# Kernel tuning notes

Measured on AMD Instinct MI355X. Metric: run time of the kernel, lower is better.

The kernel has to match this reference:

```python
import jax, jax.numpy as jnp
import numpy as np

EMB_DIM = 1024
ATTN_DIM = 1024


def setup_inputs() -> dict:
    key = jax.random.key(0)
    k_x, k_wk, k_wq, k_wv = jax.random.split(key, 4)
    bound = 1.0 / np.sqrt(EMB_DIM)  # nn.Linear default init range
    return {
        "embedded": jax.random.normal(k_x, (4, 2048, EMB_DIM), dtype=jnp.float32),
        "W_k": jax.random.uniform(k_wk, (ATTN_DIM, EMB_DIM), jnp.float32, -bound, bound),
        "W_q": jax.random.uniform(k_wq, (ATTN_DIM, EMB_DIM), jnp.float32, -bound, bound),
        "W_v": jax.random.uniform(k_wv, (ATTN_DIM, EMB_DIM), jnp.float32, -bound, bound),
    }


def reference(embedded, W_k, W_q, W_v):
    # Linear (bias=False): y = x @ W.T
    K = jnp.einsum("bse,ae->bsa", embedded, W_k)
    Q = jnp.einsum("bse,ae->bsa", embedded, W_q)
    V = jnp.einsum("bse,ae->bsa", embedded, W_v)
    S = K.shape[1]
    scale = 1.0 / jnp.sqrt(jnp.float32(ATTN_DIM))
    scores = jnp.einsum("bqa,bka->bqk", Q, K) * scale  # [B, S, S]
    causal = jnp.tril(jnp.ones((S, S), dtype=bool))  # True = keep
    scores = jnp.where(causal[None, :, :], scores, -jnp.inf)
    attn = jax.nn.softmax(scores, axis=2)
    out = jnp.einsum("bqk,bka->bqa", attn, V)
    # torch.round(x, decimals=4)
    return jnp.round(out * 1e4) / 1e4
```

## Files before the change

kernel.cpp:

```cpp
#include <hip/hip_runtime.h>
#include <stdint.h>

#define B_ 4
#define S_ 2048
#define E_ 1024
#define D_ 1024

typedef short  bf16x8 __attribute__((ext_vector_type(8)));
typedef float  f32x4  __attribute__((ext_vector_type(4)));

static __device__ __forceinline__ unsigned short f2bf(float f) {
    unsigned int u = __float_as_uint(f);
    u += 0x7fffu + ((u >> 16) & 1u);
    return (unsigned short)(u >> 16);
}

static __device__ __forceinline__ void async16(const unsigned short* g, unsigned short* l) {
    auto gp = (const __attribute__((address_space(1))) void*)(uintptr_t)g;
    auto lp = (__attribute__((address_space(3))) void*)(uintptr_t)l;
    __builtin_amdgcn_global_load_lds(gp, lp, 16, 0, 0);
}


__global__ __launch_bounds__(256)
void convert_kernel(const float* __restrict__ x,  const float* __restrict__ Wk,
                    const float* __restrict__ Wq, const float* __restrict__ Wv,
                    unsigned short* __restrict__ xb, unsigned short* __restrict__ Wb)
{
    const long long idx = ((long long)blockIdx.x * 256 + threadIdx.x) * 4;
    const float* src; unsigned short* dst; long long off;
    if (idx < (long long)B_ * S_ * E_) {
        src = x; dst = xb; off = idx;
    } else {
        long long w = idx - (long long)B_ * S_ * E_;
        const int sel = (int)(w >> 20);
        off = w & 1048575LL;
        src = (sel == 0) ? Wk : (sel == 1) ? Wq : Wv;
        dst = Wb + ((long long)sel << 20);
    }
    const float4 f = *(const float4*)(src + off);
    ushort4 u = { f2bf(f.x), f2bf(f.y), f2bf(f.z), f2bf(f.w) };
    *(ushort4*)(dst + off) = u;
}

__global__ __launch_bounds__(256, 4)
void proj_kernel(const unsigned short* __restrict__ xb,
                 const unsigned short* __restrict__ Wb,
                 unsigned short* __restrict__ Qb,
                 unsigned short* __restrict__ Kb,
                 unsigned short* __restrict__ Vt)
{
    __shared__ __align__(16) unsigned short As[128 * 64];
    __shared__ __align__(16) unsigned short Bs[128 * 64];

    const int t    = threadIdx.x;
    const int ny   = blockIdx.x;
    const int m0   = blockIdx.y * 128;
    const int wsel = ny >> 3;
    const int nloc = (ny & 7) * 128;

    const int lane = t & 63, wave = t >> 6;
    const int l15 = lane & 15, quad = lane >> 4;
    const int wm = wave & 1, wn = wave >> 1;
    const int sr = lane >> 3;
    const int sq = ((lane & 7) ^ sr) * 8;
    const int l7 = l15 & 7;
    const int rcA0 = (wm * 64 + l15) * 64 + ((quad ^ l7) * 8);
    const int rcA1 = (wm * 64 + l15) * 64 + (((4 + quad) ^ l7) * 8);
    const int rcB0 = (wn * 64 + l15) * 64 + ((quad ^ l7) * 8);
    const int rcB1 = (wn * 64 + l15) * 64 + (((4 + quad) ^ l7) * 8);

    const unsigned short* gA = xb + (size_t)(m0 + wave * 32 + sr) * E_ + sq;
    const unsigned short* gB = Wb + (size_t)(ny * 128 + wave * 32 + sr) * E_ + sq;
    unsigned short* lA = &As[wave * 2048];
    unsigned short* lB = &Bs[wave * 2048];

    f32x4 acc[4][4];
    #pragma unroll
    for (int i = 0; i < 4; i++)
        #pragma unroll
        for (int j = 0; j < 4; j++) acc[i][j] = {0.f, 0.f, 0.f, 0.f};

    for (int k0 = 0; k0 < E_; k0 += 64) {
        __syncthreads();
        #pragma unroll
        for (int i = 0; i < 4; i++) {
            async16(gA + k0 + i * 8 * E_, lA + i * 512);
            async16(gB + k0 + i * 8 * E_, lB + i * 512);
        }
        __syncthreads();

        #pragma unroll
        for (int s = 0; s < 2; s++) {
            bf16x8 af[4], bfr[4];
            const int ra = s ? rcA1 : rcA0, rb = s ? rcB1 : rcB0;
            #pragma unroll
            for (int i = 0; i < 4; i++) af[i]  = *(const bf16x8*)&As[ra + i * 1024];
            #pragma unroll
            for (int j = 0; j < 4; j++) bfr[j] = *(const bf16x8*)&Bs[rb + j * 1024];
            #pragma unroll
            for (int i = 0; i < 4; i++)
                #pragma unroll
                for (int j = 0; j < 4; j++)
                    acc[i][j] = __builtin_amdgcn_mfma_f32_16x16x32_bf16(af[i], bfr[j], acc[i][j], 0, 0, 0);
        }
    }

    if (wsel == 0) {
        #pragma unroll
        for (int i = 0; i < 4; i++)
            #pragma unroll
            for (int j = 0; j < 4; j++) {
                const int gn = nloc + wn * 64 + j * 16 + l15;
                #pragma unroll
                for (int r = 0; r < 4; r++) {
                    const int gm = m0 + wm * 64 + i * 16 + quad * 4 + r;
                    Kb[(size_t)gm * D_ + gn] = f2bf(acc[i][j][r]);
                }
            }
    } else if (wsel == 1) {
        #pragma unroll
        for (int i = 0; i < 4; i++)
            #pragma unroll
            for (int j = 0; j < 4; j++) {
                const int gn = nloc + wn * 64 + j * 16 + l15;
                #pragma unroll
                for (int r = 0; r < 4; r++) {
                    const int gm = m0 + wm * 64 + i * 16 + quad * 4 + r;
                    Qb[(size_t)gm * D_ + gn] = f2bf(acc[i][j][r] * 0.03125f);
                }
            }
    } else {
        #pragma unroll
        for (int i = 0; i < 4; i++)
            #pragma unroll
            for (int j = 0; j < 4; j++) {
                const int s0 = m0 + wm * 64 + i * 16 + quad * 4;
                const int b  = s0 >> 11, sl = s0 & (S_ - 1);
                const int gn = nloc + wn * 64 + j * 16 + l15;
                ushort4 u = { f2bf(acc[i][j][0]), f2bf(acc[i][j][1]),
                              f2bf(acc[i][j][2]), f2bf(acc[i][j][3]) };
                *(ushort4*)&Vt[((size_t)(b << 10) + gn) * S_ + sl] = u;
            }
    }
}

__global__ __launch_bounds__(256, 4)
void expscores_kernel(const unsigned short* __restrict__ Qb,
                      const unsigned short* __restrict__ Kb,
                      unsigned short* __restrict__ P,
                      float* __restrict__ rowpart)
{
    const int nt = blockIdx.x;
    const int mt = 15 - blockIdx.y;
    const int b  = blockIdx.z;
    if (nt > mt) return;

    __shared__ __align__(16) unsigned short As[128 * 64];
    __shared__ __align__(16) unsigned short Bs[128 * 64];

    const int t = threadIdx.x;
    const int m0 = mt * 128, n0 = nt * 128;

    const int lane = t & 63, wave = t >> 6;
    const int l15 = lane & 15, quad = lane >> 4;
    const int wm = wave & 1, wn = wave >> 1;
    const int sr = lane >> 3;
    const int sq = ((lane & 7) ^ sr) * 8;
    const int l7 = l15 & 7;
    const int rcA0 = (wm * 64 + l15) * 64 + ((quad ^ l7) * 8);
    const int rcA1 = (wm * 64 + l15) * 64 + (((4 + quad) ^ l7) * 8);
    const int rcB0 = (wn * 64 + l15) * 64 + ((quad ^ l7) * 8);
    const int rcB1 = (wn * 64 + l15) * 64 + (((4 + quad) ^ l7) * 8);

    const unsigned short* gA = Qb + (size_t)b * S_ * D_ + (size_t)(m0 + wave * 32 + sr) * D_ + sq;
    const unsigned short* gB = Kb + (size_t)b * S_ * D_ + (size_t)(n0 + wave * 32 + sr) * D_ + sq;
    unsigned short* lA = &As[wave * 2048];
    unsigned short* lB = &Bs[wave * 2048];

    f32x4 acc[4][4];
    #pragma unroll
    for (int i = 0; i < 4; i++)
        #pragma unroll
        for (int j = 0; j < 4; j++) acc[i][j] = {0.f, 0.f, 0.f, 0.f};

    for (int k0 = 0; k0 < D_; k0 += 64) {
        __syncthreads();
        #pragma unroll
        for (int i = 0; i < 4; i++) {
            async16(gA + k0 + i * 8 * D_, lA + i * 512);
            async16(gB + k0 + i * 8 * D_, lB + i * 512);
        }
        __syncthreads();

        #pragma unroll
        for (int s = 0; s < 2; s++) {
            bf16x8 af[4], bfr[4];
            const int ra = s ? rcA1 : rcA0, rb = s ? rcB1 : rcB0;
            #pragma unroll
            for (int i = 0; i < 4; i++) af[i]  = *(const bf16x8*)&As[ra + i * 1024];
            #pragma unroll
            for (int j = 0; j < 4; j++) bfr[j] = *(const bf16x8*)&Bs[rb + j * 1024];
            #pragma unroll
            for (int i = 0; i < 4; i++)
                #pragma unroll
                for (int j = 0; j < 4; j++)
                    acc[i][j] = __builtin_amdgcn_mfma_f32_16x16x32_bf16(af[i], bfr[j], acc[i][j], 0, 0, 0);
        }
    }

    unsigned short* Pb = P + (size_t)b * S_ * S_;
    #pragma unroll
    for (int i = 0; i < 4; i++)
        #pragma unroll
        for (int j = 0; j < 4; j++) {
            const int gn = n0 + wn * 64 + j * 16 + l15;
            #pragma unroll
            for (int r = 0; r < 4; r++) {
                const int gm = m0 + wm * 64 + i * 16 + quad * 4 + r;
                const float e = (gn <= gm) ? __expf(acc[i][j][r]) : 0.f;
                acc[i][j][r] = e;
                Pb[(size_t)gm * S_ + gn] = f2bf(e);
            }
        }

    float* rp = rowpart + ((size_t)b * 32 + nt * 2 + wn) * S_;
    #pragma unroll
    for (int i = 0; i < 4; i++) {
        float rsub[4];
        #pragma unroll
        for (int r = 0; r < 4; r++) {
            float s = acc[i][0][r] + acc[i][1][r] + acc[i][2][r] + acc[i][3][r];
            #pragma unroll
            for (int off = 8; off; off >>= 1) s += __shfl_xor(s, off);
            rsub[r] = s;
        }
        if (l15 == 0) {
            #pragma unroll
            for (int r = 0; r < 4; r++)
                rp[m0 + wm * 64 + i * 16 + quad * 4 + r] = rsub[r];
        }
    }
}

__global__ __launch_bounds__(256, 4)
void pv_kernel(const unsigned short* __restrict__ P,
               const unsigned short* __restrict__ Vt,
               const float* __restrict__ rowpart,
               float* __restrict__ out)
{
    const int nt = blockIdx.x;
    const int mt = 15 - blockIdx.y;
    const int b  = blockIdx.z;

    __shared__ __align__(16) unsigned short As[128 * 64];
    __shared__ __align__(16) unsigned short Bs[128 * 64];

    const int t = threadIdx.x;
    const int m0 = mt * 128, n0 = nt * 128;
    const int kend = m0 + 128;

    const int lane = t & 63, wave = t >> 6;
    const int l15 = lane & 15, quad = lane >> 4;
    const int wm = wave & 1, wn = wave >> 1;
    const int sr = lane >> 3;
    const int sq = ((lane & 7) ^ sr) * 8;
    const int l7 = l15 & 7;
    const int rcA0 = (wm * 64 + l15) * 64 + ((quad ^ l7) * 8);
    const int rcA1 = (wm * 64 + l15) * 64 + (((4 + quad) ^ l7) * 8);
    const int rcB0 = (wn * 64 + l15) * 64 + ((quad ^ l7) * 8);
    const int rcB1 = (wn * 64 + l15) * 64 + (((4 + quad) ^ l7) * 8);

    const unsigned short* gA = P  + (size_t)b * S_ * S_ + (size_t)(m0 + wave * 32 + sr) * S_ + sq;
    const unsigned short* gB = Vt + (size_t)b * D_ * S_ + (size_t)(n0 + wave * 32 + sr) * S_ + sq;
    unsigned short* lA = &As[wave * 2048];
    unsigned short* lB = &Bs[wave * 2048];

    f32x4 acc[4][4];
    #pragma unroll
    for (int i = 0; i < 4; i++)
        #pragma unroll
        for (int j = 0; j < 4; j++) acc[i][j] = {0.f, 0.f, 0.f, 0.f};

    for (int k0 = 0; k0 < kend; k0 += 64) {
        __syncthreads();
        #pragma unroll
        for (int i = 0; i < 4; i++) {
            async16(gA + k0 + i * 8 * S_, lA + i * 512);
            async16(gB + k0 + i * 8 * S_, lB + i * 512);
        }
        __syncthreads();

        #pragma unroll
        for (int s = 0; s < 2; s++) {
            bf16x8 af[4], bfr[4];
            const int ra = s ? rcA1 : rcA0, rb = s ? rcB1 : rcB0;
            #pragma unroll
            for (int i = 0; i < 4; i++) af[i]  = *(const bf16x8*)&As[ra + i * 1024];
            #pragma unroll
            for (int j = 0; j < 4; j++) bfr[j] = *(const bf16x8*)&Bs[rb + j * 1024];
            #pragma unroll
            for (int i = 0; i < 4; i++)
                #pragma unroll
                for (int j = 0; j < 4; j++)
                    acc[i][j] = __builtin_amdgcn_mfma_f32_16x16x32_bf16(af[i], bfr[j], acc[i][j], 0, 0, 0);
        }
    }

    const int nsl = 2 * mt + 2;
    const float* rp = rowpart + (size_t)b * 32 * S_ + (m0 + wm * 64 + lane);
    float rsum = 0.f;
    for (int k = 0; k < nsl; k++) rsum += rp[(size_t)k * S_];
    const float invr = 1.0f / rsum;

    #pragma unroll
    for (int i = 0; i < 4; i++) {
        #pragma unroll
        for (int r = 0; r < 4; r++) {
            const float vr = __shfl(invr, i * 16 + quad * 4 + r);
            const int gm = m0 + wm * 64 + i * 16 + quad * 4 + r;
            #pragma unroll
            for (int j = 0; j < 4; j++) {
                const int gn = n0 + wn * 64 + j * 16 + l15;
                out[((size_t)b * S_ + gm) * D_ + gn] = rintf(acc[i][j][r] * vr * 1e4f) * 1e-4f;
            }
        }
    }
}

extern "C" void kernel_launch(void* const* d_in, const int* in_sizes, int n_in,
                              void* d_out, int out_size, void* d_ws, size_t ws_size,
                              hipStream_t stream)
{
    (void)in_sizes; (void)n_in; (void)out_size; (void)ws_size;
    const float* x  = (const float*)d_in[0];
    const float* Wk = (const float*)d_in[1];
    const float* Wq = (const float*)d_in[2];
    const float* Wv = (const float*)d_in[3];
    float* out = (float*)d_out;

    char* ws = (char*)d_ws;
    unsigned short* Qb = (unsigned short*)ws;
    unsigned short* Kb = Qb + (size_t)B_ * S_ * D_;
    unsigned short* Vt = Kb + (size_t)B_ * S_ * D_;
    unsigned short* P  = Vt + (size_t)B_ * D_ * S_;
    unsigned short* xb = P;
    unsigned short* Wb = xb + (size_t)B_ * S_ * E_;
    float* rowpart = (float*)(P + (size_t)B_ * S_ * S_);

    const int conv_blocks = (B_ * S_ * E_ + 3 * D_ * E_) / (256 * 4);
    convert_kernel  <<<conv_blocks, 256, 0, stream>>>(x, Wk, Wq, Wv, xb, Wb);
    proj_kernel     <<<dim3(24, 64, 1),   256, 0, stream>>>(xb, Wb, Qb, Kb, Vt);
    expscores_kernel<<<dim3(16, 16, B_),  256, 0, stream>>>(Qb, Kb, P, rowpart);
    pv_kernel       <<<dim3(8, 16, B_),   256, 0, stream>>>(P, Vt, rowpart, out);
}
```

Measured before the change: 228.5 us.

## Shrink attention tiles to 64 rows and swap projection grid order

The score and PV kernels now use 64x128 tiles with 4 waves each covering 32 columns instead of 128x128 tiles, and the rowpart layout grows from 32 to 64 partial slices per row. This aims to cut wasted work on diagonal causal tiles and to give more, smaller blocks for better load balance across CUs. The cost is lower arithmetic intensity per block and more partial-sum traffic. The projection kernel's grid is also transposed so that consecutive blocks walk M rather than weight-column tiles, which changes L2 reuse of the operands.

Result: slower. 242.3 us (+6.1%).

```diff
diff --git a/kernel.cpp b/kernel.cpp
--- a/kernel.cpp
+++ b/kernel.cpp
@@ -54,8 +54,8 @@
     __shared__ __align__(16) unsigned short Bs[128 * 64];
 
     const int t    = threadIdx.x;
-    const int ny   = blockIdx.x;
-    const int m0   = blockIdx.y * 128;
+    const int m0   = blockIdx.x * 128;
+    const int ny   = blockIdx.y;
     const int wsel = ny >> 3;
     const int nloc = (ny & 7) * 128;
 
@@ -152,59 +152,58 @@
                       float* __restrict__ rowpart)
 {
     const int nt = blockIdx.x;
-    const int mt = 15 - blockIdx.y;
+    const int mt = 31 - blockIdx.y;
     const int b  = blockIdx.z;
-    if (nt > mt) return;
-
-    __shared__ __align__(16) unsigned short As[128 * 64];
+    if (nt > (mt >> 1)) return;
+
+    __shared__ __align__(16) unsigned short As[64 * 64];
     __shared__ __align__(16) unsigned short Bs[128 * 64];
 
     const int t = threadIdx.x;
-    const int m0 = mt * 128, n0 = nt * 128;
+    const int m0 = mt * 64, n0 = nt * 128;
 
     const int lane = t & 63, wave = t >> 6;
     const int l15 = lane & 15, quad = lane >> 4;
-    const int wm = wave & 1, wn = wave >> 1;
+    const int wn = wave;
     const int sr = lane >> 3;
     const int sq = ((lane & 7) ^ sr) * 8;
     const int l7 = l15 & 7;
-    const int rcA0 = (wm * 64 + l15) * 64 + ((quad ^ l7) * 8);
-    const int rcA1 = (wm * 64 + l15) * 64 + (((4 + quad) ^ l7) * 8);
-    const int rcB0 = (wn * 64 + l15) * 64 + ((quad ^ l7) * 8);
-    const int rcB1 = (wn * 64 + l15) * 64 + (((4 + quad) ^ l7) * 8);
-
-    const unsigned short* gA = Qb + (size_t)b * S_ * D_ + (size_t)(m0 + wave * 32 + sr) * D_ + sq;
+
+    const unsigned short* gA = Qb + (size_t)b * S_ * D_ + (size_t)(m0 + wave * 16 + sr) * D_ + sq;
     const unsigned short* gB = Kb + (size_t)b * S_ * D_ + (size_t)(n0 + wave * 32 + sr) * D_ + sq;
-    unsigned short* lA = &As[wave * 2048];
+    unsigned short* lA = &As[wave * 1024];
     unsigned short* lB = &Bs[wave * 2048];
 
-    f32x4 acc[4][4];
+    f32x4 acc[4][2];
     #pragma unroll
     for (int i = 0; i < 4; i++)
         #pragma unroll
-        for (int j = 0; j < 4; j++) acc[i][j] = {0.f, 0.f, 0.f, 0.f};
+        for (int j = 0; j < 2; j++) acc[i][j] = {0.f, 0.f, 0.f, 0.f};
 
     for (int k0 = 0; k0 < D_; k0 += 64) {
         __syncthreads();
         #pragma unroll
-        for (int i = 0; i < 4; i++) {
+        for (int i = 0; i < 2; i++)
             async16(gA + k0 + i * 8 * D_, lA + i * 512);
+        #pragma unroll
+        for (int i = 0; i < 4; i++)
             async16(gB + k0 + i * 8 * D_, lB + i * 512);
-        }
         __syncthreads();
 
         #pragma unroll
         for (int s = 0; s < 2; s++) {
-            bf16x8 af[4], bfr[4];
-            const int ra = s ? rcA1 : rcA0, rb = s ? rcB1 : rcB0;
-            #pragma unroll
-            for (int i = 0; i < 4; i++) af[i]  = *(const bf16x8*)&As[ra + i * 1024];
-            #pragma unroll
-            for (int j = 0; j < 4; j++) bfr[j] = *(const bf16x8*)&Bs[rb + j * 1024];
-            #pragma unroll
-            for (int i = 0; i < 4; i++)
-                #pragma unroll
-                for (int j = 0; j < 4; j++)
+            bf16x8 af[4], bfr[2];
+            const int cs = (s * 4 + quad);
+            #pragma unroll
+            for (int i = 0; i < 4; i++)
+                af[i] = *(const bf16x8*)&As[(i * 16 + l15) * 64 + ((cs ^ l7) * 8)];
+            #pragma unroll
+            for (int j = 0; j < 2; j++)
+                bfr[j] = *(const bf16x8*)&Bs[(wn * 32 + j * 16 + l15) * 64 + ((cs ^ l7) * 8)];
+            #pragma unroll
+            for (int i = 0; i < 4; i++)
+                #pragma unroll
+                for (int j = 0; j < 2; j++)
                     acc[i][j] = __builtin_amdgcn_mfma_f32_16x16x32_bf16(af[i], bfr[j], acc[i][j], 0, 0, 0);
         }
     }
@@ -213,24 +212,24 @@
     #pragma unroll
     for (int i = 0; i < 4; i++)
         #pragma unroll
-        for (int j = 0; j < 4; j++) {
-            const int gn = n0 + wn * 64 + j * 16 + l15;
+        for (int j = 0; j < 2; j++) {
+            const int gn = n0 + wn * 32 + j * 16 + l15;
             #pragma unroll
             for (int r = 0; r < 4; r++) {
-                const int gm = m0 + wm * 64 + i * 16 + quad * 4 + r;
+                const int gm = m0 + i * 16 + quad * 4 + r;
                 const float e = (gn <= gm) ? __expf(acc[i][j][r]) : 0.f;
                 acc[i][j][r] = e;
                 Pb[(size_t)gm * S_ + gn] = f2bf(e);
             }
         }
 
-    float* rp = rowpart + ((size_t)b * 32 + nt * 2 + wn) * S_;
+    float* rp = rowpart + ((size_t)b * 64 + nt * 4 + wn) * S_;
     #pragma unroll
     for (int i = 0; i < 4; i++) {
         float rsub[4];
         #pragma unroll
         for (int r = 0; r < 4; r++) {
-            float s = acc[i][0][r] + acc[i][1][r] + acc[i][2][r] + acc[i][3][r];
+            float s = acc[i][0][r] + acc[i][1][r];
             #pragma unroll
             for (int off = 8; off; off >>= 1) s += __shfl_xor(s, off);
             rsub[r] = s;
@@ -238,7 +237,7 @@
         if (l15 == 0) {
             #pragma unroll
             for (int r = 0; r < 4; r++)
-                rp[m0 + wm * 64 + i * 16 + quad * 4 + r] = rsub[r];
+                rp[m0 + i * 16 + quad * 4 + r] = rsub[r];
         }
     }
 }
@@ -250,65 +249,64 @@
                float* __restrict__ out)
 {
     const int nt = blockIdx.x;
-    const int mt = 15 - blockIdx.y;
+    const int mt = 31 - blockIdx.y;
     const int b  = blockIdx.z;
 
-    __shared__ __align__(16) unsigned short As[128 * 64];
+    __shared__ __align__(16) unsigned short As[64 * 64];
     __shared__ __align__(16) unsigned short Bs[128 * 64];
 
     const int t = threadIdx.x;
-    const int m0 = mt * 128, n0 = nt * 128;
-    const int kend = m0 + 128;
+    const int m0 = mt * 64, n0 = nt * 128;
+    const int kend = m0 + 64;
 
     const int lane = t & 63, wave = t >> 6;
     const int l15 = lane & 15, quad = lane >> 4;
-    const int wm = wave & 1, wn = wave >> 1;
+    const int wn = wave;
     const int sr = lane >> 3;
     const int sq = ((lane & 7) ^ sr) * 8;
     const int l7 = l15 & 7;
-    const int rcA0 = (wm * 64 + l15) * 64 + ((quad ^ l7) * 8);
-    const int rcA1 = (wm * 64 + l15) * 64 + (((4 + quad) ^ l7) * 8);
-    const int rcB0 = (wn * 64 + l15) * 64 + ((quad ^ l7) * 8);
-    const int rcB1 = (wn * 64 + l15) * 64 + (((4 + quad) ^ l7) * 8);
-
-    const unsigned short* gA = P  + (size_t)b * S_ * S_ + (size_t)(m0 + wave * 32 + sr) * S_ + sq;
+
+    const unsigned short* gA = P  + (size_t)b * S_ * S_ + (size_t)(m0 + wave * 16 + sr) * S_ + sq;
     const unsigned short* gB = Vt + (size_t)b * D_ * S_ + (size_t)(n0 + wave * 32 + sr) * S_ + sq;
-    unsigned short* lA = &As[wave * 2048];
+    unsigned short* lA = &As[wave * 1024];
     unsigned short* lB = &Bs[wave * 2048];
 
-    f32x4 acc[4][4];
+    f32x4 acc[4][2];
     #pragma unroll
     for (int i = 0; i < 4; i++)
         #pragma unroll
-        for (int j = 0; j < 4; j++) acc[i][j] = {0.f, 0.f, 0.f, 0.f};
+        for (int j = 0; j < 2; j++) acc[i][j] = {0.f, 0.f, 0.f, 0.f};
 
     for (int k0 = 0; k0 < kend; k0 += 64) {
         __syncthreads();
         #pragma unroll
-        for (int i = 0; i < 4; i++) {
+        for (int i = 0; i < 2; i++)
             async16(gA + k0 + i * 8 * S_, lA + i * 512);
+        #pragma unroll
+        for (int i = 0; i < 4; i++)
             async16(gB + k0 + i * 8 * S_, lB + i * 512);
-        }
         __syncthreads();
 
         #pragma unroll
         for (int s = 0; s < 2; s++) {
-            bf16x8 af[4], bfr[4];
-            const int ra = s ? rcA1 : rcA0, rb = s ? rcB1 : rcB0;
-            #pragma unroll
-            for (int i = 0; i < 4; i++) af[i]  = *(const bf16x8*)&As[ra + i * 1024];
-            #pragma unroll
-            for (int j = 0; j < 4; j++) bfr[j] = *(const bf16x8*)&Bs[rb + j * 1024];
-            #pragma unroll
-            for (int i = 0; i < 4; i++)
-                #pragma unroll
-                for (int j = 0; j < 4; j++)
+            bf16x8 af[4], bfr[2];
+            const int cs = (s * 4 + quad);
+            #pragma unroll
+            for (int i = 0; i < 4; i++)
+                af[i] = *(const bf16x8*)&As[(i * 16 + l15) * 64 + ((cs ^ l7) * 8)];
+            #pragma unroll
+            for (int j = 0; j < 2; j++)
+                bfr[j] = *(const bf16x8*)&Bs[(wn * 32 + j * 16 + l15) * 64 + ((cs ^ l7) * 8)];
+            #pragma unroll
+            for (int i = 0; i < 4; i++)
+                #pragma unroll
+                for (int j = 0; j < 2; j++)
                     acc[i][j] = __builtin_amdgcn_mfma_f32_16x16x32_bf16(af[i], bfr[j], acc[i][j], 0, 0, 0);
         }
     }
 
-    const int nsl = 2 * mt + 2;
-    const float* rp = rowpart + (size_t)b * 32 * S_ + (m0 + wm * 64 + lane);
+    const int nsl = ((mt >> 1) + 1) * 4;
+    const float* rp = rowpart + (size_t)b * 64 * S_ + (m0 + lane);
     float rsum = 0.f;
     for (int k = 0; k < nsl; k++) rsum += rp[(size_t)k * S_];
     const float invr = 1.0f / rsum;
@@ -318,10 +316,10 @@
         #pragma unroll
         for (int r = 0; r < 4; r++) {
             const float vr = __shfl(invr, i * 16 + quad * 4 + r);
-            const int gm = m0 + wm * 64 + i * 16 + quad * 4 + r;
-            #pragma unroll
-            for (int j = 0; j < 4; j++) {
-                const int gn = n0 + wn * 64 + j * 16 + l15;
+            const int gm = m0 + i * 16 + quad * 4 + r;
+            #pragma unroll
+            for (int j = 0; j < 2; j++) {
+                const int gn = n0 + wn * 32 + j * 16 + l15;
                 out[((size_t)b * S_ + gm) * D_ + gn] = rintf(acc[i][j][r] * vr * 1e4f) * 1e-4f;
             }
         }
@@ -350,7 +348,7 @@
 
     const int conv_blocks = (B_ * S_ * E_ + 3 * D_ * E_) / (256 * 4);
     convert_kernel  <<<conv_blocks, 256, 0, stream>>>(x, Wk, Wq, Wv, xb, Wb);
-    proj_kernel     <<<dim3(24, 64, 1),   256, 0, stream>>>(xb, Wb, Qb, Kb, Vt);
-    expscores_kernel<<<dim3(16, 16, B_),  256, 0, stream>>>(Qb, Kb, P, rowpart);
-    pv_kernel       <<<dim3(8, 16, B_),   256, 0, stream>>>(P, Vt, rowpart, out);
-}
+    proj_kernel     <<<dim3(64, 24, 1),   256, 0, stream>>>(xb, Wb, Qb, Kb, Vt);
+    expscores_kernel<<<dim3(16, 32, B_),  256, 0, stream>>>(Qb, Kb, P, rowpart);
+    pv_kernel       <<<dim3(8, 32, B_),   256, 0, stream>>>(P, Vt, rowpart, out);
+}
```

## Widen score and PV tiles to 128x256 and reorder projection grid

Applied to the files above, without the earlier changes.

The exp-scores and PV kernels now use 128x256 output tiles per block, with each wave computing a 64x128 sub-tile (32 accumulators). This halves the number of blocks and raises MFMA work per LDS fragment load. Row partial sums are re-indexed to 16 slices per batch, and occupancy hints drop to 2 blocks per CU. The projection grid is transposed so consecutive blocks walk M rather than N, and the expscores row order is no longer reversed. In exchange the kernels need more registers and LDS and run fewer blocks, and the 256-wide causal tiles compute more masked-out work on the diagonal.

Result: no change. 232.6 us (+1.8%).

```diff
diff --git a/kernel.cpp b/kernel.cpp
--- a/kernel.cpp
+++ b/kernel.cpp
@@ -54,8 +54,8 @@
     __shared__ __align__(16) unsigned short Bs[128 * 64];
 
     const int t    = threadIdx.x;
-    const int ny   = blockIdx.x;
-    const int m0   = blockIdx.y * 128;
+    const int m0   = blockIdx.x * 128;
+    const int ny   = blockIdx.y;
     const int wsel = ny >> 3;
     const int nloc = (ny & 7) * 128;
 
@@ -145,22 +145,22 @@
     }
 }
 
-__global__ __launch_bounds__(256, 4)
+__global__ __launch_bounds__(256, 2)
 void expscores_kernel(const unsigned short* __restrict__ Qb,
                       const unsigned short* __restrict__ Kb,
                       unsigned short* __restrict__ P,
                       float* __restrict__ rowpart)
 {
     const int nt = blockIdx.x;
-    const int mt = 15 - blockIdx.y;
+    const int mt = blockIdx.y;
     const int b  = blockIdx.z;
-    if (nt > mt) return;
+    if (nt > (mt >> 1)) return;
 
     __shared__ __align__(16) unsigned short As[128 * 64];
-    __shared__ __align__(16) unsigned short Bs[128 * 64];
+    __shared__ __align__(16) unsigned short Bs[256 * 64];
 
     const int t = threadIdx.x;
-    const int m0 = mt * 128, n0 = nt * 128;
+    const int m0 = mt * 128, n0 = nt * 256;
 
     const int lane = t & 63, wave = t >> 6;
     const int l15 = lane & 15, quad = lane >> 4;
@@ -168,43 +168,42 @@
     const int sr = lane >> 3;
     const int sq = ((lane & 7) ^ sr) * 8;
     const int l7 = l15 & 7;
-    const int rcA0 = (wm * 64 + l15) * 64 + ((quad ^ l7) * 8);
-    const int rcA1 = (wm * 64 + l15) * 64 + (((4 + quad) ^ l7) * 8);
-    const int rcB0 = (wn * 64 + l15) * 64 + ((quad ^ l7) * 8);
-    const int rcB1 = (wn * 64 + l15) * 64 + (((4 + quad) ^ l7) * 8);
 
     const unsigned short* gA = Qb + (size_t)b * S_ * D_ + (size_t)(m0 + wave * 32 + sr) * D_ + sq;
-    const unsigned short* gB = Kb + (size_t)b * S_ * D_ + (size_t)(n0 + wave * 32 + sr) * D_ + sq;
+    const unsigned short* gB = Kb + (size_t)b * S_ * D_ + (size_t)(n0 + wave * 64 + sr) * D_ + sq;
     unsigned short* lA = &As[wave * 2048];
-    unsigned short* lB = &Bs[wave * 2048];
-
-    f32x4 acc[4][4];
+    unsigned short* lB = &Bs[wave * 4096];
+
+    f32x4 acc[4][8];
     #pragma unroll
     for (int i = 0; i < 4; i++)
         #pragma unroll
-        for (int j = 0; j < 4; j++) acc[i][j] = {0.f, 0.f, 0.f, 0.f};
+        for (int j = 0; j < 8; j++) acc[i][j] = {0.f, 0.f, 0.f, 0.f};
 
     for (int k0 = 0; k0 < D_; k0 += 64) {
         __syncthreads();
         #pragma unroll
-        for (int i = 0; i < 4; i++) {
+        for (int i = 0; i < 4; i++)
             async16(gA + k0 + i * 8 * D_, lA + i * 512);
+        #pragma unroll
+        for (int i = 0; i < 8; i++)
             async16(gB + k0 + i * 8 * D_, lB + i * 512);
-        }
         __syncthreads();
 
         #pragma unroll
         for (int s = 0; s < 2; s++) {
-            bf16x8 af[4], bfr[4];
-            const int ra = s ? rcA1 : rcA0, rb = s ? rcB1 : rcB0;
-            #pragma unroll
-            for (int i = 0; i < 4; i++) af[i]  = *(const bf16x8*)&As[ra + i * 1024];
-            #pragma unroll
-            for (int j = 0; j < 4; j++) bfr[j] = *(const bf16x8*)&Bs[rb + j * 1024];
-            #pragma unroll
-            for (int i = 0; i < 4; i++)
-                #pragma unroll
-                for (int j = 0; j < 4; j++)
+            const int cs = ((s * 4 + quad) ^ l7) * 8;
+            bf16x8 af[4], bfr[8];
+            #pragma unroll
+            for (int i = 0; i < 4; i++)
+                af[i] = *(const bf16x8*)&As[(wm * 64 + i * 16 + l15) * 64 + cs];
+            #pragma unroll
+            for (int j = 0; j < 8; j++)
+                bfr[j] = *(const bf16x8*)&Bs[(wn * 128 + j * 16 + l15) * 64 + cs];
+            #pragma unroll
+            for (int i = 0; i < 4; i++)
+                #pragma unroll
+                for (int j = 0; j < 8; j++)
                     acc[i][j] = __builtin_amdgcn_mfma_f32_16x16x32_bf16(af[i], bfr[j], acc[i][j], 0, 0, 0);
         }
     }
@@ -213,8 +212,8 @@
     #pragma unroll
     for (int i = 0; i < 4; i++)
         #pragma unroll
-        for (int j = 0; j < 4; j++) {
-            const int gn = n0 + wn * 64 + j * 16 + l15;
+        for (int j = 0; j < 8; j++) {
+            const int gn = n0 + wn * 128 + j * 16 + l15;
             #pragma unroll
             for (int r = 0; r < 4; r++) {
                 const int gm = m0 + wm * 64 + i * 16 + quad * 4 + r;
@@ -224,13 +223,15 @@
             }
         }
 
-    float* rp = rowpart + ((size_t)b * 32 + nt * 2 + wn) * S_;
+    float* rp = rowpart + ((size_t)b * 16 + nt * 2 + wn) * S_;
     #pragma unroll
     for (int i = 0; i < 4; i++) {
         float rsub[4];
         #pragma unroll
         for (int r = 0; r < 4; r++) {
-            float s = acc[i][0][r] + acc[i][1][r] + acc[i][2][r] + acc[i][3][r];
+            float s = 0.f;
+            #pragma unroll
+            for (int j = 0; j < 8; j++) s += acc[i][j][r];
             #pragma unroll
             for (int off = 8; off; off >>= 1) s += __shfl_xor(s, off);
             rsub[r] = s;
@@ -243,7 +244,7 @@
     }
 }
 
-__global__ __launch_bounds__(256, 4)
+__global__ __launch_bounds__(256, 2)
 void pv_kernel(const unsigned short* __restrict__ P,
                const unsigned short* __restrict__ Vt,
                const float* __restrict__ rowpart,
@@ -254,10 +255,10 @@
     const int b  = blockIdx.z;
 
     __shared__ __align__(16) unsigned short As[128 * 64];
-    __shared__ __align__(16) unsigned short Bs[128 * 64];
+    __shared__ __align__(16) unsigned short Bs[256 * 64];
 
     const int t = threadIdx.x;
-    const int m0 = mt * 128, n0 = nt * 128;
+    const int m0 = mt * 128, n0 = nt * 256;
     const int kend = m0 + 128;
 
     const int lane = t & 63, wave = t >> 6;
@@ -266,49 +267,48 @@
     const int sr = lane >> 3;
     const int sq = ((lane & 7) ^ sr) * 8;
     const int l7 = l15 & 7;
-    const int rcA0 = (wm * 64 + l15) * 64 + ((quad ^ l7) * 8);
-    const int rcA1 = (wm * 64 + l15) * 64 + (((4 + quad) ^ l7) * 8);
-    const int rcB0 = (wn * 64 + l15) * 64 + ((quad ^ l7) * 8);
-    const int rcB1 = (wn * 64 + l15) * 64 + (((4 + quad) ^ l7) * 8);
 
     const unsigned short* gA = P  + (size_t)b * S_ * S_ + (size_t)(m0 + wave * 32 + sr) * S_ + sq;
-    const unsigned short* gB = Vt + (size_t)b * D_ * S_ + (size_t)(n0 + wave * 32 + sr) * S_ + sq;
+    const unsigned short* gB = Vt + (size_t)b * D_ * S_ + (size_t)(n0 + wave * 64 + sr) * S_ + sq;
     unsigned short* lA = &As[wave * 2048];
-    unsigned short* lB = &Bs[wave * 2048];
-
-    f32x4 acc[4][4];
+    unsigned short* lB = &Bs[wave * 4096];
+
+    f32x4 acc[4][8];
     #pragma unroll
     for (int i = 0; i < 4; i++)
         #pragma unroll
-        for (int j = 0; j < 4; j++) acc[i][j] = {0.f, 0.f, 0.f, 0.f};
+        for (int j = 0; j < 8; j++) acc[i][j] = {0.f, 0.f, 0.f, 0.f};
 
     for (int k0 = 0; k0 < kend; k0 += 64) {
         __syncthreads();
         #pragma unroll
-        for (int i = 0; i < 4; i++) {
+        for (int i = 0; i < 4; i++)
             async16(gA + k0 + i * 8 * S_, lA + i * 512);
+        #pragma unroll
+        for (int i = 0; i < 8; i++)
             async16(gB + k0 + i * 8 * S_, lB + i * 512);
-        }
         __syncthreads();
 
         #pragma unroll
         for (int s = 0; s < 2; s++) {
-            bf16x8 af[4], bfr[4];
-            const int ra = s ? rcA1 : rcA0, rb = s ? rcB1 : rcB0;
-            #pragma unroll
-            for (int i = 0; i < 4; i++) af[i]  = *(const bf16x8*)&As[ra + i * 1024];
-            #pragma unroll
-            for (int j = 0; j < 4; j++) bfr[j] = *(const bf16x8*)&Bs[rb + j * 1024];
-            #pragma unroll
-            for (int i = 0; i < 4; i++)
-                #pragma unroll
-                for (int j = 0; j < 4; j++)
+            const int cs = ((s * 4 + quad) ^ l7) * 8;
+            bf16x8 af[4], bfr[8];
+            #pragma unroll
+            for (int i = 0; i < 4; i++)
+                af[i] = *(const bf16x8*)&As[(wm * 64 + i * 16 + l15) * 64 + cs];
+            #pragma unroll
+            for (int j = 0; j < 8; j++)
+                bfr[j] = *(const bf16x8*)&Bs[(wn * 128 + j * 16 + l15) * 64 + cs];
+            #pragma unroll
+            for (int i = 0; i < 4; i++)
+                #pragma unroll
+                for (int j = 0; j < 8; j++)
                     acc[i][j] = __builtin_amdgcn_mfma_f32_16x16x32_bf16(af[i], bfr[j], acc[i][j], 0, 0, 0);
         }
     }
 
-    const int nsl = 2 * mt + 2;
-    const float* rp = rowpart + (size_t)b * 32 * S_ + (m0 + wm * 64 + lane);
+    const int nsl = 2 * ((mt >> 1) + 1);
+    const float* rp = rowpart + (size_t)b * 16 * S_ + (m0 + wm * 64 + lane);
     float rsum = 0.f;
     for (int k = 0; k < nsl; k++) rsum += rp[(size_t)k * S_];
     const float invr = 1.0f / rsum;
@@ -320,8 +320,8 @@
             const float vr = __shfl(invr, i * 16 + quad * 4 + r);
             const int gm = m0 + wm * 64 + i * 16 + quad * 4 + r;
             #pragma unroll
-            for (int j = 0; j < 4; j++) {
-                const int gn = n0 + wn * 64 + j * 16 + l15;
+            for (int j = 0; j < 8; j++) {
+                const int gn = n0 + wn * 128 + j * 16 + l15;
                 out[((size_t)b * S_ + gm) * D_ + gn] = rintf(acc[i][j][r] * vr * 1e4f) * 1e-4f;
             }
         }
@@ -350,7 +350,7 @@
 
     const int conv_blocks = (B_ * S_ * E_ + 3 * D_ * E_) / (256 * 4);
     convert_kernel  <<<conv_blocks, 256, 0, stream>>>(x, Wk, Wq, Wv, xb, Wb);
-    proj_kernel     <<<dim3(24, 64, 1),   256, 0, stream>>>(xb, Wb, Qb, Kb, Vt);
-    expscores_kernel<<<dim3(16, 16, B_),  256, 0, stream>>>(Qb, Kb, P, rowpart);
-    pv_kernel       <<<dim3(8, 16, B_),   256, 0, stream>>>(P, Vt, rowpart, out);
-}
+    proj_kernel     <<<dim3(64, 24, 1),   256, 0, stream>>>(xb, Wb, Qb, Kb, Vt);
+    expscores_kernel<<<dim3(8, 16, B_),   256, 0, stream>>>(Qb, Kb, P, rowpart);
+    pv_kernel       <<<dim3(4, 16, B_),   256, 0, stream>>>(P, Vt, rowpart, out);
+}
```
